# Kernel optimization log

Hardware: AMD Instinct MI355X
Metric: run time of the kernel (lower is better)

Reference implementation:

```python
import jax, jax.numpy as jnp
import numpy as np

B, N, DIM_IN, DIM_OUT, EMBED, CHEB_K = 32, 2000, 64, 64, 16, 3


def setup_inputs() -> dict:
    key = jax.random.key(0)
    ks = jax.random.split(key, 6)
    return {
        "x": jax.random.normal(ks[0], (B, N, DIM_IN), dtype=jnp.float32),
        "node_embeddings": jax.random.normal(ks[1], (N, EMBED), dtype=jnp.float32),
        "nodevec1": jax.random.normal(ks[2], (N, EMBED), dtype=jnp.float32),
        "nodevec2": jax.random.normal(ks[3], (EMBED, N), dtype=jnp.float32),
        "weights_pool": jax.random.normal(ks[4], (EMBED, CHEB_K, DIM_IN, DIM_OUT), dtype=jnp.float32) * 0.1,
        "bias_pool": jax.random.normal(ks[5], (EMBED, DIM_OUT), dtype=jnp.float32) * 0.1,
    }


def reference(x, node_embeddings, nodevec1, nodevec2, weights_pool, bias_pool):
    n = node_embeddings.shape[0]
    # adaptive adjacency: softmax(relu(nodevec1 @ nodevec2)) over rows' neighbors
    s = jax.nn.softmax(jax.nn.relu(nodevec1 @ nodevec2), axis=1)  # [N, N]
    # Chebyshev polynomial stack: T0 = I, T1 = S, Tk = 2 S Tk-1 - Tk-2
    support_set = [jnp.eye(n, dtype=x.dtype), s]
    for _ in range(2, CHEB_K):
        support_set.append(2.0 * s @ support_set[-1] - support_set[-2])
    supports = jnp.stack(support_set, axis=0)  # [K, N, N]
    # node-conditioned weights / bias
    weights = jnp.einsum('nd,dkio->nkio', node_embeddings, weights_pool)  # [N, K, I, O]
    bias = node_embeddings @ bias_pool  # [N, O]
    # graph conv: aggregate then per-node combine
    x_g = jnp.einsum('knm,bmc->bnkc', supports, x)  # [B, N, K, I]
    out = jnp.einsum('bnki,nkio->bno', x_g, weights) + bias  # [B, N, O]
    return out
```

## Files before the change

### kernel.cpp

```cpp
#include <hip/hip_runtime.h>

#define N_NODES 2000
#define NP      2048
#define KB      63
#define KB3     66
#define BATCH   32
#define DIM     64
#define EMB     16
#define KI      192
#define WCOLS   12288

typedef __bf16 bf16;
typedef __attribute__((ext_vector_type(8))) __bf16 bf16x8;
typedef __attribute__((ext_vector_type(4))) float  f32x4;

struct alignas(8) bf16x4pk { bf16 v[4]; };

__device__ __forceinline__ void gl_lds16(const bf16* g, bf16* l) {
    __builtin_amdgcn_global_load_lds(
        (__attribute__((address_space(1))) void*)(g),
        (__attribute__((address_space(3))) void*)(l), 16, 0, 0);
}


#define Z0   (WCOLS * 32)
#define Z1   (Z0 + N_NODES * 32)
#define Z2   (Z1 + 3 * NP * 32)
#define PREP_SM_BLK   2554
#define PREP_BLOCKS   (N_NODES + 1024 + PREP_SM_BLK)

#define PW_BLOCKS 1200

__global__ __launch_bounds__(256) void prep_fused(
    const float* __restrict__ nv1, const float* __restrict__ nv2,
    bf16* __restrict__ Sp,
    const float* __restrict__ X, bf16* __restrict__ Xtp, bf16* __restrict__ Xbf,
    const float* __restrict__ wp, const float* __restrict__ emb,
    bf16* __restrict__ wpT2, bf16* __restrict__ embp, bf16* __restrict__ Sp63)
{
    const int bid = blockIdx.x;
    const int tid = threadIdx.x;

    if (bid < N_NODES) {
        const int row = bid;
        const int j0  = tid * 8;
        __shared__ float sa[EMB];
        __shared__ float wred[4];
        __shared__ float bcast;
        if (tid < EMB) sa[tid] = nv1[row * EMB + tid];
        __syncthreads();

        const bool active = (tid < 250);
        float v[8] = {0,0,0,0,0,0,0,0};
        if (active) {
#pragma unroll
            for (int d = 0; d < EMB; ++d) {
                const float sd = sa[d];
                const float4 q0 = *(const float4*)&nv2[d * N_NODES + j0];
                const float4 q1 = *(const float4*)&nv2[d * N_NODES + j0 + 4];
                v[0] += sd * q0.x; v[1] += sd * q0.y; v[2] += sd * q0.z; v[3] += sd * q0.w;
                v[4] += sd * q1.x; v[5] += sd * q1.y; v[6] += sd * q1.z; v[7] += sd * q1.w;
            }
        }
        float lmax = 0.0f;
#pragma unroll
        for (int jj = 0; jj < 8; ++jj) { v[jj] = fmaxf(v[jj], 0.0f); lmax = fmaxf(lmax, v[jj]); }
#pragma unroll
        for (int off = 32; off > 0; off >>= 1)
            lmax = fmaxf(lmax, __shfl_down(lmax, off, 64));
        if ((tid & 63) == 0) wred[tid >> 6] = lmax;
        __syncthreads();
        if (tid == 0) bcast = fmaxf(fmaxf(wred[0], wred[1]), fmaxf(wred[2], wred[3]));
        __syncthreads();
        const float rmax = bcast;

        float lsum = 0.0f;
        if (active) {
#pragma unroll
            for (int jj = 0; jj < 8; ++jj) { v[jj] = __expf(v[jj] - rmax); lsum += v[jj]; }
        }
#pragma unroll
        for (int off = 32; off > 0; off >>= 1)
            lsum += __shfl_down(lsum, off, 64);
        if ((tid & 63) == 0) wred[tid >> 6] = lsum;
        __syncthreads();
        if (tid == 0) bcast = wred[0] + wred[1] + wred[2] + wred[3];
        __syncthreads();
        const float inv = 1.0f / bcast;

        if (tid < 252) {
            bf16x8 pk;
#pragma unroll
            for (int jj = 0; jj < 8; ++jj)
                pk[jj] = (bf16)(active ? v[jj] * inv : 0.0f);
            const int kb = j0 >> 5, q = (j0 >> 3) & 3;
            const int nt = row >> 6, r = row & 63;
            *(bf16x8*)&Sp[((size_t)(kb * 32 + nt) * 256 + q * 64 + r) * 8] = pk;
        }
    } else if (bid < N_NODES + 1024) {
        const int t  = bid - N_NODES;
        const int b  = t >> 5;
        const int m0 = (t & 31) * 64;
        __shared__ bf16 T[64][72];
#pragma unroll
        for (int i = 0; i < 4; ++i) {
            int idx = i * 256 + tid;
            int r  = idx >> 4;
            int c4 = (idx & 15) * 4;
            int m  = m0 + r;
            float4 v = make_float4(0.f, 0.f, 0.f, 0.f);
            if (m < N_NODES)
                v = *(const float4*)&X[((size_t)b * N_NODES + m) * DIM + c4];
            bf16x4pk pk;
            pk.v[0] = (bf16)v.x; pk.v[1] = (bf16)v.y;
            pk.v[2] = (bf16)v.z; pk.v[3] = (bf16)v.w;
            if (m < N_NODES)
                *(bf16x4pk*)&Xbf[((size_t)b * N_NODES + m) * DIM + c4] = pk;
            T[c4 + 0][r] = pk.v[0];
            T[c4 + 1][r] = pk.v[1];
            T[c4 + 2][r] = pk.v[2];
            T[c4 + 3][r] = pk.v[3];
        }
        __syncthreads();
#pragma unroll
        for (int i = 0; i < 2; ++i) {
            int idx = i * 256 + tid;
            int c   = idx >> 3;
            int mch = idx & 7;
            int kb  = (m0 >> 5) + (mch >> 2);
            if (kb < KB) {
                int q = mch & 3;
                bf16x8 vv = *(const bf16x8*)&T[c][mch * 8];
                *(bf16x8*)&Xtp[((size_t)(b * KB3 + kb) * 256 + q * 64 + c) * 8] = vv;
            }
        }
    } else {
        int idx = (bid - N_NODES - 1024) * 256 + tid;
        if (idx < Z0) {
            int col = idx >> 5, d = idx & 31;
            int o  = col / KI;
            int kk = col - o * KI;
            int cheb = kk >> 6, i = kk & 63;
            float v = (d < EMB) ? wp[(((d * 3 + cheb) * 64 + i) * 64) + o] : 0.0f;
            wpT2[idx] = (bf16)v;
        } else if (idx < Z1) {
            int j = idx - Z0;
            int n = j >> 5, d = j & 31;
            float v = (d < EMB) ? emb[n * EMB + d] : 0.0f;
            embp[j] = (bf16)v;
        } else if (idx < Z2) {
            Sp63[idx - Z1] = (bf16)0.0f;
        }
    }
}

__global__ __launch_bounds__(256, 3) void spmm_pipe4(
    const bf16* __restrict__ Ap, const bf16* __restrict__ Btp,
    bf16* __restrict__ Ybf, bf16* __restrict__ Ytp,
    const bf16* __restrict__ embp, const bf16* __restrict__ wpT2,
    bf16* __restrict__ W, int write_ytp)
{
    __shared__ __align__(16) char smem[49152];
    const int bid  = blockIdx.x;
    const int tid  = threadIdx.x;
    const int lane = tid & 63, wave = tid >> 6;
    const int l15  = lane & 15, quad = lane >> 4;

    if (bid < 512) {
        bf16* As = (bf16*)smem;
        bf16* Bs = (bf16*)(smem + 32768);

        const int kx = bid & 7, j = bid >> 3;
        const int ntB = (j & 7) + 8 * (kx & 1);
        const int b   = ((j >> 3) << 2) + (kx >> 1);
        const int n0  = ntB * 128;

        const bf16* aslab = Ap  + (size_t)(ntB * 2) * 2048 + tid * 8;
        const bf16* bslab = Btp + (size_t)(b * KB3) * 2048 + tid * 8;

#define STAGE(buf, s_) {                                               \
        const bf16* pa = aslab + (size_t)(s_) * (32 * 2048);           \
        const bf16* pb = bslab + (size_t)(s_) * 2048;                  \
        gl_lds16(pa,        &As[(buf) * 4096 + tid * 8]);              \
        gl_lds16(pa + 2048, &As[(buf) * 4096 + 2048 + tid * 8]);       \
        gl_lds16(pb,        &Bs[(buf) * 2048 + tid * 8]); }

        f32x4 acc[2][4] = {};
        const int ga = (wave >> 1) * 256 + quad * 64 + (wave & 1) * 32;
        const int gb = quad * 64;

        STAGE(0, 0);
        STAGE(1, 1);
        STAGE(2, 2);
#pragma unroll 1
        for (int s = 0; s < 66; ++s) {
            const int cur = s & 3;
            if (s < 64) {
                asm volatile("s_waitcnt vmcnt(6)" ::: "memory");
            } else if (s == 64) {
                asm volatile("s_waitcnt vmcnt(3)" ::: "memory");
            } else {
                asm volatile("s_waitcnt vmcnt(0)" ::: "memory");
            }
            __builtin_amdgcn_s_barrier();
            __builtin_amdgcn_sched_barrier(0);
            if (s + 3 < 66) STAGE((s + 3) & 3, s + 3);
            bf16x8 af[2], bfr[4];
#pragma unroll
            for (int t = 0; t < 2; ++t)
                af[t]  = *(const bf16x8*)&As[cur * 4096 + (ga + t * 16 + l15) * 8];
#pragma unroll
            for (int t = 0; t < 4; ++t)
                bfr[t] = *(const bf16x8*)&Bs[cur * 2048 + (gb + t * 16 + l15) * 8];
#pragma unroll
            for (int rt = 0; rt < 2; ++rt)
#pragma unroll
                for (int ct = 0; ct < 4; ++ct)
                    acc[rt][ct] = __builtin_amdgcn_mfma_f32_16x16x32_bf16(
                        af[rt], bfr[ct], acc[rt][ct], 0, 0, 0);
        }
#undef STAGE

#pragma unroll
        for (int rt = 0; rt < 2; ++rt) {
            const int nbase = n0 + wave * 32 + rt * 16 + quad * 4;
#pragma unroll
            for (int ct = 0; ct < 4; ++ct) {
                const int c = ct * 16 + l15;
#pragma unroll
                for (int r = 0; r < 4; ++r) {
                    int n = nbase + r;
                    if (n < N_NODES)
                        Ybf[((size_t)b * N_NODES + n) * DIM + c] = (bf16)acc[rt][ct][r];
                }
                if (write_ytp && nbase + 4 <= N_NODES) {
                    const int kb2 = nbase >> 5;
                    const int kq  = (nbase & 31) >> 3;
                    const int j4  = nbase & 7;
                    bf16x4pk pk;
                    pk.v[0] = (bf16)acc[rt][ct][0];
                    pk.v[1] = (bf16)acc[rt][ct][1];
                    pk.v[2] = (bf16)acc[rt][ct][2];
                    pk.v[3] = (bf16)acc[rt][ct][3];
                    *(bf16x4pk*)&Ytp[((size_t)(b * KB3 + kb2) * 256 + kq * 64 + c) * 8 + j4] = pk;
                }
            }
        }
    } else {
        bf16 (*Cs)[264] = (bf16(*)[264])smem;

        const int pid     = bid - 512;
        const int colbase = (pid % 48) * 256;
        const int ng0     = (pid / 48) * 5;

        bf16x8 bfr[4];
#pragma unroll
        for (int ct = 0; ct < 4; ++ct) {
            const int col = colbase + wave * 64 + ct * 16 + l15;
            bfr[ct] = *(const bf16x8*)&wpT2[(size_t)col * 32 + quad * 8];
        }
        bf16x8 afs[5];
#pragma unroll
        for (int g = 0; g < 5; ++g)
            afs[g] = *(const bf16x8*)&embp[(size_t)((ng0 + g) * 16 + l15) * 32 + quad * 8];
        const f32x4 zero = {};

#pragma unroll
        for (int g = 0; g < 5; ++g) {
            const int n0 = (ng0 + g) * 16;
#pragma unroll
            for (int ct = 0; ct < 4; ++ct) {
                f32x4 acc = __builtin_amdgcn_mfma_f32_16x16x32_bf16(afs[g], bfr[ct], zero, 0, 0, 0);
#pragma unroll
                for (int r = 0; r < 4; ++r)
                    Cs[quad * 4 + r][wave * 64 + ct * 16 + l15] = (bf16)acc[r];
            }
            __syncthreads();
            {
                const int row = tid >> 4;
                const int c16 = (tid & 15) * 16;
                bf16x8 v0 = *(const bf16x8*)&Cs[row][c16];
                bf16x8 v1 = *(const bf16x8*)&Cs[row][c16 + 8];
                bf16* dst = &W[(size_t)(n0 + row) * WCOLS + colbase + c16];
                *(bf16x8*)dst       = v0;
                *(bf16x8*)(dst + 8) = v1;
            }
            __syncthreads();
        }
    }
}

__global__ __launch_bounds__(256) void combine_node(
    const bf16* __restrict__ xbf, const bf16* __restrict__ y1bf,
    const bf16* __restrict__ y2bf, const float* __restrict__ emb,
    const float* __restrict__ bp, const bf16* __restrict__ W,
    float* __restrict__ out)
{
    const int n   = blockIdx.x;
    const int tid = threadIdx.x;
    const int lane = tid & 63, wave = tid >> 6;
    const int l15 = lane & 15, quad = lane >> 4;

    __shared__ bf16 As[BATCH][200];
    __shared__ bf16 Ws[DIM][200];
    __shared__ float bias_s[DIM];
    __shared__ float emb_s[EMB];

    if (tid < EMB) emb_s[tid] = emb[n * EMB + tid];

    {
        const int b  = tid >> 3;
        const int c8 = (tid & 7) * 8;
        const size_t base = ((size_t)b * N_NODES + n) * DIM + c8;
        bf16x8 vx = *(const bf16x8*)&xbf [base];
        bf16x8 v1 = *(const bf16x8*)&y1bf[base];
        bf16x8 v2 = *(const bf16x8*)&y2bf[base];
        bf16x8 p2;
#pragma unroll
        for (int e = 0; e < 8; ++e)
            p2[e] = (bf16)(2.0f * (float)v2[e] - (float)vx[e]);
        *(bf16x8*)&As[b][c8]       = vx;
        *(bf16x8*)&As[b][64 + c8]  = v1;
        *(bf16x8*)&As[b][128 + c8] = p2;
    }
    {
        const bf16* Wn = W + (size_t)n * WCOLS;
#pragma unroll
        for (int jj = 0; jj < 6; ++jj) {
            int chunk = jj * 256 + tid;
            int o  = chunk / 24;
            int kc = chunk - o * 24;
            bf16x8 v = *(const bf16x8*)&Wn[(size_t)chunk * 8];
            *(bf16x8*)&Ws[o][kc * 8] = v;
        }
    }
    __syncthreads();

    if (tid < DIM) {
        float s = 0.0f;
#pragma unroll
        for (int d = 0; d < EMB; ++d) s += emb_s[d] * bp[d * DIM + tid];
        bias_s[tid] = s;
    }

    bf16x8 af[2][6];
#pragma unroll
    for (int mt = 0; mt < 2; ++mt)
#pragma unroll
        for (int ks = 0; ks < 6; ++ks)
            af[mt][ks] = *(const bf16x8*)&As[mt * 16 + l15][ks * 32 + quad * 8];

    f32x4 acc[2] = {};
#pragma unroll
    for (int ks = 0; ks < 6; ++ks) {
        bf16x8 bfr = *(const bf16x8*)&Ws[wave * 16 + l15][ks * 32 + quad * 8];
        acc[0] = __builtin_amdgcn_mfma_f32_16x16x32_bf16(af[0][ks], bfr, acc[0], 0, 0, 0);
        acc[1] = __builtin_amdgcn_mfma_f32_16x16x32_bf16(af[1][ks], bfr, acc[1], 0, 0, 0);
    }
    __syncthreads();

    const int o = wave * 16 + l15;
    const float bv = bias_s[o];
#pragma unroll
    for (int mt = 0; mt < 2; ++mt)
#pragma unroll
        for (int r = 0; r < 4; ++r) {
            int b = mt * 16 + quad * 4 + r;
            out[((size_t)b * N_NODES + n) * DIM + o] = acc[mt][r] + bv;
        }
}

extern "C" void kernel_launch(void* const* d_in, const int* in_sizes, int n_in,
                              void* d_out, int out_size, void* d_ws, size_t ws_size,
                              hipStream_t stream) {
    const float* x   = (const float*)d_in[0];
    const float* emb = (const float*)d_in[1];
    const float* nv1 = (const float*)d_in[2];
    const float* nv2 = (const float*)d_in[3];
    const float* wp  = (const float*)d_in[4];
    const float* bp  = (const float*)d_in[5];
    float* out = (float*)d_out;

    char* w = (char*)d_ws;
    bf16* Sp   = (bf16*)w;  w += (size_t)KB3 * NP * 32 * 2;
    bf16* xTp  = (bf16*)w;  w += (size_t)BATCH * KB3 * DIM * 32 * 2;
    bf16* y1Tp = (bf16*)w;  w += (size_t)BATCH * KB3 * DIM * 32 * 2;
    bf16* xbf  = (bf16*)w;  w += (size_t)BATCH * N_NODES * DIM * 2;
    bf16* y1bf = (bf16*)w;  w += (size_t)BATCH * N_NODES * DIM * 2;
    bf16* y2bf = (bf16*)w;  w += (size_t)BATCH * N_NODES * DIM * 2;
    bf16* wpT2 = (bf16*)w;  w += (size_t)WCOLS * 32 * 2;
    bf16* embp = (bf16*)w;  w += (size_t)N_NODES * 32 * 2;
    bf16* W    = (bf16*)w;

    prep_fused<<<PREP_BLOCKS, 256, 0, stream>>>(
        nv1, nv2, Sp, x, xTp, xbf, wp, emb, wpT2, embp,
        Sp + (size_t)63 * NP * 32);
    spmm_pipe4<<<512 + PW_BLOCKS, 256, 0, stream>>>(Sp, xTp, y1bf, y1Tp, embp, wpT2, W, 1);
    spmm_pipe4<<<512, 256, 0, stream>>>(Sp, y1Tp, y2bf, y1Tp, embp, wpT2, W, 0);
    combine_node<<<N_NODES, 256, 0, stream>>>(xbf, y1bf, y2bf, emb, bp, W, out);
}
```

Measured before the change: 165.3 us.

## Replace LDS-staged SPMM pipeline with direct register double-buffered global loads

The S·X GEMM no longer stages A and B tiles through LDS with global_load_lds and a 4-deep barrier pipeline. Each wave now loads its MFMA fragments straight from global memory into registers and prefetches the next k-step while computing the current one. This removes LDS traffic and per-step block barriers, and frees shared memory that may raise occupancy. In exchange, fragments that several waves share (the B tile and A rows) are loaded redundantly from global/L2, and latency hiding is only one step deep.

```diff
diff --git a/kernel.cpp b/kernel.cpp
--- a/kernel.cpp
+++ b/kernel.cpp
@@ -15,12 +15,6 @@
 typedef __attribute__((ext_vector_type(4))) float  f32x4;
 
 struct alignas(8) bf16x4pk { bf16 v[4]; };
-
-__device__ __forceinline__ void gl_lds16(const bf16* g, bf16* l) {
-    __builtin_amdgcn_global_load_lds(
-        (__attribute__((address_space(1))) void*)(g),
-        (__attribute__((address_space(3))) void*)(l), 16, 0, 0);
-}
 
 
 #define Z0   (WCOLS * 32)
@@ -154,76 +148,68 @@
     }
 }
 
-__global__ __launch_bounds__(256, 3) void spmm_pipe4(
+__global__ __launch_bounds__(256, 3) void spmm_reg(
     const bf16* __restrict__ Ap, const bf16* __restrict__ Btp,
     bf16* __restrict__ Ybf, bf16* __restrict__ Ytp,
     const bf16* __restrict__ embp, const bf16* __restrict__ wpT2,
     bf16* __restrict__ W, int write_ytp)
 {
-    __shared__ __align__(16) char smem[49152];
     const int bid  = blockIdx.x;
     const int tid  = threadIdx.x;
     const int lane = tid & 63, wave = tid >> 6;
     const int l15  = lane & 15, quad = lane >> 4;
 
     if (bid < 512) {
-        bf16* As = (bf16*)smem;
-        bf16* Bs = (bf16*)(smem + 32768);
-
         const int kx = bid & 7, j = bid >> 3;
         const int ntB = (j & 7) + 8 * (kx & 1);
         const int b   = ((j >> 3) << 2) + (kx >> 1);
         const int n0  = ntB * 128;
 
-        const bf16* aslab = Ap  + (size_t)(ntB * 2) * 2048 + tid * 8;
-        const bf16* bslab = Btp + (size_t)(b * KB3) * 2048 + tid * 8;
-
-#define STAGE(buf, s_) {                                               \
-        const bf16* pa = aslab + (size_t)(s_) * (32 * 2048);           \
-        const bf16* pb = bslab + (size_t)(s_) * 2048;                  \
-        gl_lds16(pa,        &As[(buf) * 4096 + tid * 8]);              \
-        gl_lds16(pa + 2048, &As[(buf) * 4096 + 2048 + tid * 8]);       \
-        gl_lds16(pb,        &Bs[(buf) * 2048 + tid * 8]); }
+        const bf16* aptr = Ap + ((size_t)(ntB * 2 + (wave >> 1)) * 256
+                                 + quad * 64 + (wave & 1) * 32 + l15) * 8;
+        const bf16* bptr = Btp + ((size_t)(b * KB3) * 256
+                                  + quad * 64 + l15) * 8;
 
         f32x4 acc[2][4] = {};
-        const int ga = (wave >> 1) * 256 + quad * 64 + (wave & 1) * 32;
-        const int gb = quad * 64;
-
-        STAGE(0, 0);
-        STAGE(1, 1);
-        STAGE(2, 2);
-#pragma unroll 1
+
+        bf16x8 A0, A1, B0, B1, B2, B3;
+        {
+            A0 = *(const bf16x8*)(aptr);
+            A1 = *(const bf16x8*)(aptr + 128);
+            B0 = *(const bf16x8*)(bptr);
+            B1 = *(const bf16x8*)(bptr + 128);
+            B2 = *(const bf16x8*)(bptr + 256);
+            B3 = *(const bf16x8*)(bptr + 384);
+        }
+#pragma unroll 2
         for (int s = 0; s < 66; ++s) {
-            const int cur = s & 3;
-            if (s < 64) {
-                asm volatile("s_waitcnt vmcnt(6)" ::: "memory");
-            } else if (s == 64) {
-                asm volatile("s_waitcnt vmcnt(3)" ::: "memory");
-            } else {
-                asm volatile("s_waitcnt vmcnt(0)" ::: "memory");
-            }
-            __builtin_amdgcn_s_barrier();
-            __builtin_amdgcn_sched_barrier(0);
-            if (s + 3 < 66) STAGE((s + 3) & 3, s + 3);
-            bf16x8 af[2], bfr[4];
-#pragma unroll
-            for (int t = 0; t < 2; ++t)
-                af[t]  = *(const bf16x8*)&As[cur * 4096 + (ga + t * 16 + l15) * 8];
-#pragma unroll
-            for (int t = 0; t < 4; ++t)
-                bfr[t] = *(const bf16x8*)&Bs[cur * 2048 + (gb + t * 16 + l15) * 8];
-#pragma unroll
-            for (int rt = 0; rt < 2; ++rt)
-#pragma unroll
-                for (int ct = 0; ct < 4; ++ct)
-                    acc[rt][ct] = __builtin_amdgcn_mfma_f32_16x16x32_bf16(
-                        af[rt], bfr[ct], acc[rt][ct], 0, 0, 0);
-        }
-#undef STAGE
+            bf16x8 nA0, nA1, nB0, nB1, nB2, nB3;
+            if (s + 1 < 66) {
+                const bf16* pa = aptr + (size_t)(s + 1) * 65536;
+                const bf16* pb = bptr + (size_t)(s + 1) * 2048;
+                nA0 = *(const bf16x8*)(pa);
+                nA1 = *(const bf16x8*)(pa + 128);
+                nB0 = *(const bf16x8*)(pb);
+                nB1 = *(const bf16x8*)(pb + 128);
+                nB2 = *(const bf16x8*)(pb + 256);
+                nB3 = *(const bf16x8*)(pb + 384);
+            }
+            acc[0][0] = __builtin_amdgcn_mfma_f32_16x16x32_bf16(A0, B0, acc[0][0], 0, 0, 0);
+            acc[0][1] = __builtin_amdgcn_mfma_f32_16x16x32_bf16(A0, B1, acc[0][1], 0, 0, 0);
+            acc[0][2] = __builtin_amdgcn_mfma_f32_16x16x32_bf16(A0, B2, acc[0][2], 0, 0, 0);
+            acc[0][3] = __builtin_amdgcn_mfma_f32_16x16x32_bf16(A0, B3, acc[0][3], 0, 0, 0);
+            acc[1][0] = __builtin_amdgcn_mfma_f32_16x16x32_bf16(A1, B0, acc[1][0], 0, 0, 0);
+            acc[1][1] = __builtin_amdgcn_mfma_f32_16x16x32_bf16(A1, B1, acc[1][1], 0, 0, 0);
+            acc[1][2] = __builtin_amdgcn_mfma_f32_16x16x32_bf16(A1, B2, acc[1][2], 0, 0, 0);
+            acc[1][3] = __builtin_amdgcn_mfma_f32_16x16x32_bf16(A1, B3, acc[1][3], 0, 0, 0);
+            A0 = nA0; A1 = nA1;
+            B0 = nB0; B1 = nB1; B2 = nB2; B3 = nB3;
+        }
 
 #pragma unroll
         for (int rt = 0; rt < 2; ++rt) {
-            const int nbase = n0 + wave * 32 + rt * 16 + quad * 4;
+            const int nbase = n0 + (wave >> 1) * 64 + (wave & 1) * 32
+                              + rt * 16 + quad * 4;
 #pragma unroll
             for (int ct = 0; ct < 4; ++ct) {
                 const int c = ct * 16 + l15;
@@ -247,7 +233,7 @@
             }
         }
     } else {
-        bf16 (*Cs)[264] = (bf16(*)[264])smem;
+        __shared__ bf16 Cs[16][264];
 
         const int pid     = bid - 512;
         const int colbase = (pid % 48) * 256;
@@ -395,7 +381,7 @@
     prep_fused<<<PREP_BLOCKS, 256, 0, stream>>>(
         nv1, nv2, Sp, x, xTp, xbf, wp, emb, wpT2, embp,
         Sp + (size_t)63 * NP * 32);
-    spmm_pipe4<<<512 + PW_BLOCKS, 256, 0, stream>>>(Sp, xTp, y1bf, y1Tp, embp, wpT2, W, 1);
-    spmm_pipe4<<<512, 256, 0, stream>>>(Sp, y1Tp, y2bf, y1Tp, embp, wpT2, W, 0);
+    spmm_reg<<<512 + PW_BLOCKS, 256, 0, stream>>>(Sp, xTp, y1bf, y1Tp, embp, wpT2, W, 1);
+    spmm_reg<<<512, 256, 0, stream>>>(Sp, y1Tp, y2bf, y1Tp, embp, wpT2, W, 0);
     combine_node<<<N_NODES, 256, 0, stream>>>(xbf, y1bf, y2bf, emb, bp, W, out);
 }
```

New measurement: 172.7 us. +4.5%, slower.
